# Kernel optimization log

Hardware: AMD Instinct MI355X
Metric: run time of the kernel (lower is better)

Reference implementation:

```python
import jax, jax.numpy as jnp
import numpy as np

B, N, FIN, D = 4, 16384, 128, 256
GX, GY = 32, 32
M = GX * GY
NBR = 1
K = (2 * NBR + 1) ** 2
IMG_W, IMG_H = 256.0, 256.0
CELL_W, CELL_H = IMG_W / GX, IMG_H / GY
EPS = 1e-5

# (K,2) offsets, row-major (-n,-n)..(n,n), [dx,dy] like torch _build_offsets_2d
_ys, _xs = np.meshgrid(np.arange(-NBR, NBR + 1), np.arange(-NBR, NBR + 1), indexing='ij')
OFFSETS = jnp.asarray(np.stack([_xs.ravel(), _ys.ravel()], axis=-1), dtype=jnp.int32)  # (K,2)


def setup_inputs() -> dict:
    key = jax.random.key(0)
    ks = jax.random.split(key, 16)
    s = 0.02
    return {
        'features': jax.random.normal(ks[0], (B, N, FIN), dtype=jnp.float32),
        'coords': jax.random.uniform(ks[1], (B, N, 2), dtype=jnp.float32) * IMG_W,
        'valid_mask': jnp.ones((B, N), dtype=bool),
        'Wf': jax.random.normal(ks[2], (FIN, D), dtype=jnp.float32) * s,
        'bf': jnp.zeros((D,), dtype=jnp.float32),
        'Wq': jax.random.normal(ks[3], (D, D), dtype=jnp.float32) * s,
        'bq': jnp.zeros((D,), dtype=jnp.float32),
        'Wk': jax.random.normal(ks[4], (D, D), dtype=jnp.float32) * s,
        'bk': jnp.zeros((D,), dtype=jnp.float32),
        'Wv': jax.random.normal(ks[5], (D, D), dtype=jnp.float32) * s,
        'bv': jnp.zeros((D,), dtype=jnp.float32),
        'Wo': jax.random.normal(ks[6], (D, D), dtype=jnp.float32) * s,
        'bo': jnp.zeros((D,), dtype=jnp.float32),
        'pos_emb': jax.random.normal(ks[7], (K, D), dtype=jnp.float32) * s,
        'gamma': jnp.ones((D,), dtype=jnp.float32),
        'beta': jnp.zeros((D,), dtype=jnp.float32),
    }


def _forward(features, coords, valid_mask, Wf, bf, Wq, bq, Wk, bk, Wv, bv, Wo, bo, pos_emb, gamma, beta):
    feat = features @ Wf + bf  # (B,N,D)

    # coords -> grid cell indices (truncation == torch .long() for nonneg coords)
    ix = jnp.clip((coords[..., 0] / CELL_W).astype(jnp.int32), 0, GX - 1)
    iy = jnp.clip((coords[..., 1] / CELL_H).astype(jnp.int32), 0, GY - 1)
    lin = ix * GY + iy  # (B,N)

    # scatter-mean pool into grid cells
    base = (jnp.arange(B, dtype=jnp.int32) * M)[:, None]
    gid = (lin + base).reshape(-1)  # (B*N,)
    pooled = jax.ops.segment_sum(feat.reshape(-1, D), gid, num_segments=B * M)
    cnt = jax.ops.segment_sum(jnp.ones((B * N,), feat.dtype), gid, num_segments=B * M)
    grid_flat = (pooled / jnp.maximum(cnt, 1.0)[:, None]).reshape(B, M, D)

    # neighbor gather with edge clamping + validity mask
    nbx = ix[:, :, None] + OFFSETS[None, None, :, 0]  # (B,N,K)
    nby = iy[:, :, None] + OFFSETS[None, None, :, 1]
    valid = (nbx >= 0) & (nbx < GX) & (nby >= 0) & (nby < GY)
    lin_n = jnp.clip(nbx, 0, GX - 1) * GY + jnp.clip(nby, 0, GY - 1)  # (B,N,K)
    nbr_feat = jnp.take_along_axis(grid_flat, lin_n.reshape(B, N * K, 1), axis=1).reshape(B, N, K, D)
    nbr_feat = nbr_feat + pos_emb[None, None, :, :]

    # tiny-window attention (1 query vs K neighbors); SDPA scale = 1/sqrt(D)
    Q = feat @ Wq + bq  # (B,N,D)
    Kt = nbr_feat @ Wk + bk  # (B,N,K,D)
    Vt = nbr_feat @ Wv + bv
    scores = jnp.einsum('bnd,bnkd->bnk', Q, Kt) / jnp.sqrt(jnp.float32(D))
    scores = jnp.where(valid, scores, -jnp.inf)
    attn = jax.nn.softmax(scores, axis=-1)
    out = jnp.einsum('bnk,bnkd->bnd', attn, Vt)
    out = out @ Wo + bo

    # residual + layernorm
    h = feat + out
    mu = jnp.mean(h, axis=-1, keepdims=True)
    var = jnp.var(h, axis=-1, keepdims=True)
    h = (h - mu) * jax.lax.rsqrt(var + EPS) * gamma + beta

    return jnp.where(valid_mask[..., None], h, feat)


def reference(features, coords, valid_mask, Wf, bf, Wq, bq, Wk, bk, Wv, bv, Wo, bo, pos_emb, gamma, beta):
    return _forward(features, coords, valid_mask, Wf, bf, Wq, bq, Wk, bk, Wv, bv, Wo, bo, pos_emb, gamma, beta)
```

## Files before the change

### kernel.cpp

```cpp
#include <hip/hip_runtime.h>
#include <math.h>

typedef _Float16 f16;
typedef _Float16 f16x8 __attribute__((ext_vector_type(8)));
typedef float f32x4 __attribute__((ext_vector_type(4)));

constexpr int cB   = 4;
constexpr int cN   = 16384;
constexpr int cFIN = 128;
constexpr int cD   = 256;
constexpr int cGX  = 32;
constexpr int cGY  = 32;
constexpr int cM   = cGX * cGY;
constexpr int cBM  = cB * cM;
constexpr int cBN  = cB * cN;
constexpr int cK   = 9;
constexpr float cEPS = 1e-5f;
constexpr int RPB  = 64;
constexpr int GSTR = 264;
constexpr int FSTR = 264;

struct f16pair { f16 h; f16 l; };
__device__ inline f16pair split2(float x) {
  f16pair p;
  p.h = (f16)x;
  p.l = (f16)(x - (float)p.h);
  return p;
}

__global__ __launch_bounds__(256)
void k_index(const float* __restrict__ coords, int* __restrict__ lin_arr,
             int* __restrict__ cntI) {
  int p = blockIdx.x * 256 + threadIdx.x;
  if (p >= cBN) return;
  float x = coords[2 * p], y = coords[2 * p + 1];
  int ix = (int)(x * 0.125f);
  int iy = (int)(y * 0.125f);
  ix = min(max(ix, 0), cGX - 1);
  iy = min(max(iy, 0), cGY - 1);
  int lin = ix * cGY + iy;
  lin_arr[p] = lin;
  int b = p / cN;
  atomicAdd(&cntI[b * cM + lin], 1);
}

__global__ __launch_bounds__(1024)
void k_scan(const int* __restrict__ cntI, int* __restrict__ bstart,
            int* __restrict__ bfill) {
  __shared__ int sums[1024];
  int t = threadIdx.x;
  int base = t * 4;
  int v0 = cntI[base], v1 = cntI[base + 1], v2 = cntI[base + 2], v3 = cntI[base + 3];
  sums[t] = v0 + v1 + v2 + v3;
  __syncthreads();
  for (int off = 1; off < 1024; off <<= 1) {
    int val = (t >= off) ? sums[t - off] : 0;
    __syncthreads();
    sums[t] += val;
    __syncthreads();
  }
  int run = (t == 0) ? 0 : sums[t - 1];
  bstart[base] = run;     bfill[base] = run;     run += v0;
  bstart[base + 1] = run; bfill[base + 1] = run; run += v1;
  bstart[base + 2] = run; bfill[base + 2] = run; run += v2;
  bstart[base + 3] = run; bfill[base + 3] = run; run += v3;
  if (t == 1023) bstart[4096] = run;
}

__global__ __launch_bounds__(256)
void k_scatteridx(const int* __restrict__ lin_arr, int* __restrict__ bfill,
                  int* __restrict__ sorted) {
  int p = blockIdx.x * 256 + threadIdx.x;
  if (p >= cBN) return;
  int b = p / cN;
  int gid = b * cM + lin_arr[p];
  int pos = atomicAdd(&bfill[gid], 1);
  sorted[pos] = p;
}

__global__ __launch_bounds__(256)
void k_precompute(const float* __restrict__ Wf, const float* __restrict__ Wq,
                  const float* __restrict__ Wv, const float* __restrict__ Wo,
                  const float* __restrict__ Wk, const float* __restrict__ pe,
                  const float* __restrict__ bf, const float* __restrict__ bq,
                  const float* __restrict__ bv, const float* __restrict__ bo,
                  const float* __restrict__ bk,
                  f16* __restrict__ BTh, f16* __restrict__ BTl,
                  f16* __restrict__ WvoTh, f16* __restrict__ WvoTl,
                  f16* __restrict__ WkTh, f16* __restrict__ WkTl,
                  float* __restrict__ bias2, float* __restrict__ bvo,
                  float* __restrict__ PK, float* __restrict__ PVO) {
  __shared__ float sA[cD];
  __shared__ float sB[cD];
  int bid = blockIdx.x, n = threadIdx.x;
  if (bid < cFIN) {
    int k = bid;
    f16pair pw = split2(Wf[k * cD + n]);
    BTh[n * cFIN + k] = pw.h; BTl[n * cFIN + k] = pw.l;
    float acc = 0.f;
    for (int c = 0; c < cD; c++) acc += Wf[k * cD + c] * Wq[c * cD + n];
    f16pair p = split2(acc);
    BTh[(256 + n) * cFIN + k] = p.h;
    BTl[(256 + n) * cFIN + k] = p.l;
  } else if (bid < cFIN + cD) {
    int k = bid - cFIN;
    float acc = 0.f;
    for (int c = 0; c < cD; c++) acc += Wv[k * cD + c] * Wo[c * cD + n];
    f16pair p = split2(acc);
    WvoTh[n * cD + k] = p.h;
    WvoTl[n * cD + k] = p.l;
  } else if (bid == cFIN + cD) {
    float aq = 0.f, ao = 0.f;
    for (int c = 0; c < cD; c++) {
      aq += bf[c] * Wq[c * cD + n];
      ao += bv[c] * Wo[c * cD + n];
    }
    bias2[n] = bf[n];
    bias2[256 + n] = aq + bq[n];
    bvo[n] = ao + bo[n];
  } else if (bid < cFIN + cD + 1 + cD) {
    int n2 = bid - (cFIN + cD + 1);
    f16pair p = split2(Wk[n * cD + n2]);
    WkTh[n2 * cD + n] = p.h;
    WkTl[n2 * cD + n] = p.l;
  } else {
    int k = bid - (cFIN + cD + 1 + cD);
    sA[n] = pe[k * cD + n];
    __syncthreads();
    float av = 0.f, ak = 0.f;
    for (int c = 0; c < cD; c++) {
      float pv = sA[c];
      av += pv * Wv[c * cD + n];
      ak += pv * Wk[c * cD + n];
    }
    sB[n] = av;
    PK[k * cD + n] = ak + bk[n];
    __syncthreads();
    float ao = 0.f;
    for (int c = 0; c < cD; c++) ao += sB[c] * Wo[c * cD + n];
    PVO[k * cD + n] = ao;
  }
}

__global__ __launch_bounds__(256)
void k_poolsum(const float* __restrict__ features, const int* __restrict__ sorted,
               const int* __restrict__ bstart, f16* __restrict__ Sh,
               f16* __restrict__ Sl, f16* __restrict__ Fh, f16* __restrict__ Fl) {
  __shared__ float Stmp[2][cFIN];
  int gid = blockIdx.x;
  int t = threadIdx.x;
  int half = t >> 7, ch = t & 127;
  int s0 = bstart[gid], s1 = bstart[gid + 1];
  float acc = 0.f;
  for (int i = s0 + half; i < s1; i += 2) {
    int srow = sorted[i];
    float v = features[(size_t)srow * cFIN + ch];
    acc += v;
    f16pair pp = split2(v);
    Fh[(size_t)srow * cFIN + ch] = pp.h;
    Fl[(size_t)srow * cFIN + ch] = pp.l;
  }
  Stmp[half][ch] = acc;
  __syncthreads();
  if (half == 0) {
    f16pair p = split2(Stmp[0][ch] + Stmp[1][ch]);
    Sh[(size_t)gid * cFIN + ch] = p.h;
    Sl[(size_t)gid * cFIN + ch] = p.l;
  }
}

__global__ __launch_bounds__(256)
void k_gemm_gkv(const f16* __restrict__ Sh, const f16* __restrict__ Sl,
                const f16* __restrict__ WfTh, const f16* __restrict__ WfTl,
                const float* __restrict__ bfp, const int* __restrict__ bstart,
                const f16* __restrict__ WkTh, const f16* __restrict__ WkTl,
                const f16* __restrict__ WvoTh, const f16* __restrict__ WvoTl,
                float* __restrict__ GK, float* __restrict__ GVO) {
  __shared__ f16 gshH[RPB * GSTR];
  __shared__ f16 gshL[RPB * GSTR];
  int t = threadIdx.x;
  int w = t >> 6, lane = t & 63;
  int q = lane >> 4, l = lane & 15;
  size_t row0 = (size_t)blockIdx.x * RPB;

  f32x4 acc[4][4];
#pragma unroll
  for (int rs = 0; rs < 4; rs++)
#pragma unroll
    for (int tc = 0; tc < 4; tc++) acc[rs][tc] = (f32x4){0.f, 0.f, 0.f, 0.f};

  for (int kk = 0; kk < cFIN; kk += 32) {
    f16x8 a_h[4], a_l[4];
#pragma unroll
    for (int rs = 0; rs < 4; rs++) {
      size_t aoff = (row0 + rs * 16 + l) * cFIN + q * 8 + kk;
      a_h[rs] = *(const f16x8*)(Sh + aoff);
      a_l[rs] = *(const f16x8*)(Sl + aoff);
    }
#pragma unroll
    for (int tc = 0; tc < 4; tc++) {
      size_t boff = (size_t)((w * 4 + tc) * 16 + l) * cFIN + q * 8 + kk;
      f16x8 bh = *(const f16x8*)(WfTh + boff);
      f16x8 bl = *(const f16x8*)(WfTl + boff);
#pragma unroll
      for (int rs = 0; rs < 4; rs++) {
        acc[rs][tc] = __builtin_amdgcn_mfma_f32_16x16x32_f16(a_h[rs], bh, acc[rs][tc], 0, 0, 0);
        acc[rs][tc] = __builtin_amdgcn_mfma_f32_16x16x32_f16(a_h[rs], bl, acc[rs][tc], 0, 0, 0);
        acc[rs][tc] = __builtin_amdgcn_mfma_f32_16x16x32_f16(a_l[rs], bh, acc[rs][tc], 0, 0, 0);
      }
    }
  }
#pragma unroll
  for (int tc = 0; tc < 4; tc++) {
    int col = (w * 4 + tc) * 16 + l;
    float bias = bfp[col];
#pragma unroll
    for (int rs = 0; rs < 4; rs++)
#pragma unroll
      for (int r = 0; r < 4; r++) {
        size_t row = row0 + rs * 16 + q * 4 + r;
        int lr = rs * 16 + q * 4 + r;
        int cnt = bstart[row + 1] - bstart[row];
        float g = (cnt > 0) ? (acc[rs][tc][r] / (float)cnt + bias) : 0.f;
        f16pair p = split2(g);
        gshH[lr * GSTR + col] = p.h;
        gshL[lr * GSTR + col] = p.l;
      }
  }
  __syncthreads();

  for (int sel = 0; sel < 2; sel++) {
    const f16* BTh = sel ? WvoTh : WkTh;
    const f16* BTl = sel ? WvoTl : WkTl;
    float* outp = sel ? GVO : GK;
#pragma unroll
    for (int rs = 0; rs < 4; rs++)
#pragma unroll
      for (int tc = 0; tc < 4; tc++) acc[rs][tc] = (f32x4){0.f, 0.f, 0.f, 0.f};
    for (int kk = 0; kk < cD; kk += 32) {
      f16x8 a_h[4], a_l[4];
#pragma unroll
      for (int rs = 0; rs < 4; rs++) {
        int aoff = (rs * 16 + l) * GSTR + q * 8 + kk;
        a_h[rs] = *(const f16x8*)(gshH + aoff);
        a_l[rs] = *(const f16x8*)(gshL + aoff);
      }
#pragma unroll
      for (int tc = 0; tc < 4; tc++) {
        size_t boff = (size_t)((w * 4 + tc) * 16 + l) * cD + q * 8 + kk;
        f16x8 bh = *(const f16x8*)(BTh + boff);
        f16x8 bl = *(const f16x8*)(BTl + boff);
#pragma unroll
        for (int rs = 0; rs < 4; rs++) {
          acc[rs][tc] = __builtin_amdgcn_mfma_f32_16x16x32_f16(a_h[rs], bh, acc[rs][tc], 0, 0, 0);
          acc[rs][tc] = __builtin_amdgcn_mfma_f32_16x16x32_f16(a_h[rs], bl, acc[rs][tc], 0, 0, 0);
          acc[rs][tc] = __builtin_amdgcn_mfma_f32_16x16x32_f16(a_l[rs], bh, acc[rs][tc], 0, 0, 0);
        }
      }
    }
#pragma unroll
    for (int tc = 0; tc < 4; tc++) {
      int col = (w * 4 + tc) * 16 + l;
#pragma unroll
      for (int rs = 0; rs < 4; rs++)
#pragma unroll
        for (int r = 0; r < 4; r++) {
          size_t row = row0 + rs * 16 + q * 4 + r;
          outp[row * cD + col] = acc[rs][tc][r];
        }
    }
  }
}

__global__ __launch_bounds__(256)
void k_gemmFQ(const f16* __restrict__ Fh, const f16* __restrict__ Fl,
              const f16* __restrict__ BTh, const f16* __restrict__ BTl,
              const float* __restrict__ bias2,
              float* __restrict__ feat_out, float* __restrict__ Qout) {
  __shared__ float sC[16 * FSTR];
  int y = blockIdx.y;
  int t = threadIdx.x;
  int w = t >> 6, lane = t & 63;
  int q = lane >> 4, l = lane & 15;
  size_t row0 = (size_t)blockIdx.x * RPB;
  float* outp = y ? Qout : feat_out;

  f32x4 acc[4][4];
#pragma unroll
  for (int rs = 0; rs < 4; rs++)
#pragma unroll
    for (int tc = 0; tc < 4; tc++) acc[rs][tc] = (f32x4){0.f, 0.f, 0.f, 0.f};

  for (int kk = 0; kk < cFIN; kk += 32) {
    f16x8 a_h[4], a_l[4];
#pragma unroll
    for (int rs = 0; rs < 4; rs++) {
      size_t aoff = (row0 + rs * 16 + l) * cFIN + q * 8 + kk;
      a_h[rs] = *(const f16x8*)(Fh + aoff);
      a_l[rs] = *(const f16x8*)(Fl + aoff);
    }
#pragma unroll
    for (int tc = 0; tc < 4; tc++) {
      int ct = y * 16 + w * 4 + tc;
      size_t boff = (size_t)(ct * 16 + l) * cFIN + q * 8 + kk;
      f16x8 bh = *(const f16x8*)(BTh + boff);
      f16x8 bl = *(const f16x8*)(BTl + boff);
#pragma unroll
      for (int rs = 0; rs < 4; rs++) {
        acc[rs][tc] = __builtin_amdgcn_mfma_f32_16x16x32_f16(a_h[rs], bh, acc[rs][tc], 0, 0, 0);
        acc[rs][tc] = __builtin_amdgcn_mfma_f32_16x16x32_f16(a_h[rs], bl, acc[rs][tc], 0, 0, 0);
        acc[rs][tc] = __builtin_amdgcn_mfma_f32_16x16x32_f16(a_l[rs], bh, acc[rs][tc], 0, 0, 0);
      }
    }
  }

#pragma unroll
  for (int rs = 0; rs < 4; rs++) {
    if (rs > 0) __syncthreads();
#pragma unroll
    for (int tc = 0; tc < 4; tc++) {
      int col = (w * 4 + tc) * 16 + l;
      float b = bias2[y * 256 + col];
#pragma unroll
      for (int r = 0; r < 4; r++)
        sC[(q * 4 + r) * FSTR + col] = acc[rs][tc][r] + b;
    }
    __syncthreads();
#pragma unroll
    for (int j = 0; j < 4; j++) {
      int idx = j * 256 + t;
      int lr = idx >> 6;
      int c4 = (idx & 63) * 4;
      *(float4*)&outp[(row0 + rs * 16 + lr) * cD + c4] =
          *(const float4*)&sC[lr * FSTR + c4];
    }
  }
}

__global__ __launch_bounds__(256)
void k_attn(const float* __restrict__ Qbuf, const float* __restrict__ GK,
            const float* __restrict__ GVO, const float* __restrict__ PK,
            const float* __restrict__ PVO, const int* __restrict__ sorted,
            const int* __restrict__ bstart, const float* __restrict__ bvop,
            const float* __restrict__ gammap, const float* __restrict__ betap,
            float* __restrict__ out) {
  __shared__ float KK[cK][cD];
  __shared__ float VV[cK][cD];
  int gid = blockIdx.x;
  int b = gid / cM;
  int lin = gid % cM;
  int ix = lin / cGY, iy = lin % cGY;
  int t = threadIdx.x;

  int vm = 0;
  for (int k = 0; k < cK; k++) {
    int dx = k % 3 - 1, dy = k / 3 - 1;
    int nx = ix + dx, ny = iy + dy;
    bool v = (nx >= 0 && nx < cGX && ny >= 0 && ny < cGY);
    if (v) vm |= (1 << k);
    int cx = min(max(nx, 0), cGX - 1);
    int cy = min(max(ny, 0), cGY - 1);
    size_t nlin = (size_t)(b * cM + cx * cGY + cy);
    KK[k][t] = GK[nlin * cD + t] + PK[k * cD + t];
    VV[k][t] = GVO[nlin * cD + t] + PVO[k * cD + t];
  }
  __syncthreads();

  int s0 = bstart[gid], s1 = bstart[gid + 1];
  int wv = t >> 6, lane = t & 63;
  float4 c4 = *(const float4*)&bvop[lane * 4];
  float4 g4 = *(const float4*)&gammap[lane * 4];
  float4 be4 = *(const float4*)&betap[lane * 4];

  int ip = s0 + wv;
  if (ip >= s1) return;
  int p = sorted[ip];
  size_t off0 = (size_t)p * cD + lane * 4;
  float4 q4 = *(const float4*)&Qbuf[off0];
  float4 f = *(const float4*)&out[off0];
  while (true) {
    int ipn = ip + 4;
    bool more = ipn < s1;
    int pn = 0; size_t offn = 0;
    float4 q4n = {0.f, 0.f, 0.f, 0.f}, fn = {0.f, 0.f, 0.f, 0.f};
    if (more) {
      pn = sorted[ipn];
      offn = (size_t)pn * cD + lane * 4;
      q4n = *(const float4*)&Qbuf[offn];
      fn = *(const float4*)&out[offn];
    }

    float sc[cK];
#pragma unroll
    for (int k = 0; k < cK; k++) {
      float4 kk = *(const float4*)&KK[k][lane * 4];
      sc[k] = q4.x * kk.x + q4.y * kk.y + q4.z * kk.z + q4.w * kk.w;
    }
#pragma unroll
    for (int off = 32; off > 0; off >>= 1)
#pragma unroll
      for (int k = 0; k < cK; k++) sc[k] += __shfl_xor(sc[k], off, 64);

    float mx = -1e30f;
#pragma unroll
    for (int k = 0; k < cK; k++)
      if ((vm >> k) & 1) mx = fmaxf(mx, sc[k] * 0.0625f);
    float e[cK], ssum = 0.f;
#pragma unroll
    for (int k = 0; k < cK; k++) {
      float v = ((vm >> k) & 1) ? __expf(sc[k] * 0.0625f - mx) : 0.f;
      e[k] = v; ssum += v;
    }
    float inv = 1.f / ssum;
    float4 o = {0.f, 0.f, 0.f, 0.f};
#pragma unroll
    for (int k = 0; k < cK; k++) {
      float a = e[k] * inv;
      float4 vv = *(const float4*)&VV[k][lane * 4];
      o.x += a * vv.x; o.y += a * vv.y; o.z += a * vv.z; o.w += a * vv.w;
    }
    float4 h;
    h.x = f.x + o.x + c4.x; h.y = f.y + o.y + c4.y;
    h.z = f.z + o.z + c4.z; h.w = f.w + o.w + c4.w;
    float s = h.x + h.y + h.z + h.w;
    float ss = h.x * h.x + h.y * h.y + h.z * h.z + h.w * h.w;
#pragma unroll
    for (int o2 = 32; o2 > 0; o2 >>= 1) {
      s += __shfl_xor(s, o2, 64);
      ss += __shfl_xor(ss, o2, 64);
    }
    float mu = s * (1.f / cD);
    float var = ss * (1.f / cD) - mu * mu;
    float rs = rsqrtf(var + cEPS);
    float4 r;
    r.x = (h.x - mu) * rs * g4.x + be4.x;
    r.y = (h.y - mu) * rs * g4.y + be4.y;
    r.z = (h.z - mu) * rs * g4.z + be4.z;
    r.w = (h.w - mu) * rs * g4.w + be4.w;
    *(float4*)&out[off0] = r;

    if (!more) break;
    ip = ipn; p = pn; off0 = offn; q4 = q4n; f = fn;
  }
}

extern "C" void kernel_launch(void* const* d_in, const int* in_sizes, int n_in,
                              void* d_out, int out_size, void* d_ws, size_t ws_size,
                              hipStream_t stream) {
  (void)in_sizes; (void)n_in; (void)out_size; (void)ws_size;
  const float* features = (const float*)d_in[0];
  const float* coords   = (const float*)d_in[1];
  const float* Wf = (const float*)d_in[3];
  const float* bf = (const float*)d_in[4];
  const float* Wq = (const float*)d_in[5];
  const float* bq = (const float*)d_in[6];
  const float* Wk = (const float*)d_in[7];
  const float* bk = (const float*)d_in[8];
  const float* Wv = (const float*)d_in[9];
  const float* bv = (const float*)d_in[10];
  const float* Wo = (const float*)d_in[11];
  const float* bo = (const float*)d_in[12];
  const float* pe = (const float*)d_in[13];
  const float* gm = (const float*)d_in[14];
  const float* bt = (const float*)d_in[15];
  float* out = (float*)d_out;

  char* ws = (char*)d_ws;
  size_t o = 0;
  auto take = [&](size_t bytes) -> void* {
    void* p = ws + o;
    o = (o + bytes + 255) & ~(size_t)255;
    return p;
  };
  int* lin_arr = (int*)take((size_t)cBN * 4);
  int* sorted  = (int*)take((size_t)cBN * 4);
  int* bstart  = (int*)take((size_t)(cBM + 1) * 4);
  int* bfill   = (int*)take((size_t)cBM * 4);
  int* cntI    = (int*)take((size_t)cBM * 4);
  float* GK    = (float*)take((size_t)cBM * cD * 4);
  float* GVO   = (float*)take((size_t)cBM * cD * 4);
  float* PK    = (float*)take((size_t)cK * cD * 4);
  float* PVO   = (float*)take((size_t)cK * cD * 4);
  float* Qbuf  = (float*)take((size_t)cBN * cD * 4);
  f16* Fh      = (f16*)take((size_t)cBN * cFIN * 2);
  f16* Fl      = (f16*)take((size_t)cBN * cFIN * 2);
  f16* BTh     = (f16*)take((size_t)512 * cFIN * 2);
  f16* BTl     = (f16*)take((size_t)512 * cFIN * 2);
  f16* WvoTh   = (f16*)take((size_t)cD * cD * 2);
  f16* WvoTl   = (f16*)take((size_t)cD * cD * 2);
  f16* WkTh    = (f16*)take((size_t)cD * cD * 2);
  f16* WkTl    = (f16*)take((size_t)cD * cD * 2);
  f16* Sh      = (f16*)take((size_t)cBM * cFIN * 2);
  f16* Sl      = (f16*)take((size_t)cBM * cFIN * 2);
  float* bias2 = (float*)take((size_t)512 * 4);
  float* bvo   = (float*)take((size_t)cD * 4);

  (void)hipMemsetAsync(cntI, 0, (size_t)cBM * 4, stream);

  k_index<<<cBN / 256, 256, 0, stream>>>(coords, lin_arr, cntI);
  k_scan<<<1, 1024, 0, stream>>>(cntI, bstart, bfill);
  k_scatteridx<<<cBN / 256, 256, 0, stream>>>(lin_arr, bfill, sorted);
  k_precompute<<<cFIN + cD + 1 + cD + cK, 256, 0, stream>>>(
      Wf, Wq, Wv, Wo, Wk, pe, bf, bq, bv, bo, bk,
      BTh, BTl, WvoTh, WvoTl, WkTh, WkTl, bias2, bvo, PK, PVO);
  k_poolsum<<<cBM, 256, 0, stream>>>(features, sorted, bstart, Sh, Sl, Fh, Fl);
  k_gemm_gkv<<<cBM / RPB, 256, 0, stream>>>(Sh, Sl, BTh, BTl, bf, bstart,
                                            WkTh, WkTl, WvoTh, WvoTl, GK, GVO);
  dim3 gFQ(cBN / RPB, 2);
  k_gemmFQ<<<gFQ, 256, 0, stream>>>(Fh, Fl, BTh, BTl, bias2, out, Qbuf);
  k_attn<<<cBM, 256, 0, stream>>>(Qbuf, GK, GVO, PK, PVO, sorted, bstart,
                                  bvo, gm, bt, out);
}
```

Before: 334.6 us.

## Shrink grid GEMM tiles, prefetch A in FQ GEMM, use half-wave rows in attention

The grid-cell GEMM now processes 16 rows per block instead of 64, giving 256 blocks instead of 64 so more CUs are busy on this small GEMM, at the cost of reloading weight tiles more often. The feature/Q GEMM double-buffers its A-operand loads across K steps to hide global latency. The attention kernel maps each point to a 32-lane half-wave handling 8 channels per lane, processing 8 points per block at a time with shorter shuffle reductions. The sC row stride padding also changes from 264 to 268.

```diff
diff --git a/kernel.cpp b/kernel.cpp
--- a/kernel.cpp
+++ b/kernel.cpp
@@ -17,8 +17,9 @@
 constexpr int cK   = 9;
 constexpr float cEPS = 1e-5f;
 constexpr int RPB  = 64;
+constexpr int RPG  = 16;
 constexpr int GSTR = 264;
-constexpr int FSTR = 264;
+constexpr int FSTR = 268;
 
 struct f16pair { f16 h; f16 l; };
 __device__ inline f16pair split2(float x) {
@@ -176,38 +177,29 @@
                 const f16* __restrict__ WkTh, const f16* __restrict__ WkTl,
                 const f16* __restrict__ WvoTh, const f16* __restrict__ WvoTl,
                 float* __restrict__ GK, float* __restrict__ GVO) {
-  __shared__ f16 gshH[RPB * GSTR];
-  __shared__ f16 gshL[RPB * GSTR];
+  __shared__ f16 gshH[RPG * GSTR];
+  __shared__ f16 gshL[RPG * GSTR];
   int t = threadIdx.x;
   int w = t >> 6, lane = t & 63;
   int q = lane >> 4, l = lane & 15;
-  size_t row0 = (size_t)blockIdx.x * RPB;
-
-  f32x4 acc[4][4];
-#pragma unroll
-  for (int rs = 0; rs < 4; rs++)
-#pragma unroll
-    for (int tc = 0; tc < 4; tc++) acc[rs][tc] = (f32x4){0.f, 0.f, 0.f, 0.f};
+  size_t row0 = (size_t)blockIdx.x * RPG;
+
+  f32x4 acc[4];
+#pragma unroll
+  for (int tc = 0; tc < 4; tc++) acc[tc] = (f32x4){0.f, 0.f, 0.f, 0.f};
 
   for (int kk = 0; kk < cFIN; kk += 32) {
-    f16x8 a_h[4], a_l[4];
-#pragma unroll
-    for (int rs = 0; rs < 4; rs++) {
-      size_t aoff = (row0 + rs * 16 + l) * cFIN + q * 8 + kk;
-      a_h[rs] = *(const f16x8*)(Sh + aoff);
-      a_l[rs] = *(const f16x8*)(Sl + aoff);
-    }
+    size_t aoff = (row0 + l) * cFIN + q * 8 + kk;
+    f16x8 a_h = *(const f16x8*)(Sh + aoff);
+    f16x8 a_l = *(const f16x8*)(Sl + aoff);
 #pragma unroll
     for (int tc = 0; tc < 4; tc++) {
       size_t boff = (size_t)((w * 4 + tc) * 16 + l) * cFIN + q * 8 + kk;
       f16x8 bh = *(const f16x8*)(WfTh + boff);
       f16x8 bl = *(const f16x8*)(WfTl + boff);
-#pragma unroll
-      for (int rs = 0; rs < 4; rs++) {
-        acc[rs][tc] = __builtin_amdgcn_mfma_f32_16x16x32_f16(a_h[rs], bh, acc[rs][tc], 0, 0, 0);
-        acc[rs][tc] = __builtin_amdgcn_mfma_f32_16x16x32_f16(a_h[rs], bl, acc[rs][tc], 0, 0, 0);
-        acc[rs][tc] = __builtin_amdgcn_mfma_f32_16x16x32_f16(a_l[rs], bh, acc[rs][tc], 0, 0, 0);
-      }
+      acc[tc] = __builtin_amdgcn_mfma_f32_16x16x32_f16(a_h, bh, acc[tc], 0, 0, 0);
+      acc[tc] = __builtin_amdgcn_mfma_f32_16x16x32_f16(a_h, bl, acc[tc], 0, 0, 0);
+      acc[tc] = __builtin_amdgcn_mfma_f32_16x16x32_f16(a_l, bh, acc[tc], 0, 0, 0);
     }
   }
 #pragma unroll
@@ -215,17 +207,15 @@
     int col = (w * 4 + tc) * 16 + l;
     float bias = bfp[col];
 #pragma unroll
-    for (int rs = 0; rs < 4; rs++)
-#pragma unroll
-      for (int r = 0; r < 4; r++) {
-        size_t row = row0 + rs * 16 + q * 4 + r;
-        int lr = rs * 16 + q * 4 + r;
-        int cnt = bstart[row + 1] - bstart[row];
-        float g = (cnt > 0) ? (acc[rs][tc][r] / (float)cnt + bias) : 0.f;
-        f16pair p = split2(g);
-        gshH[lr * GSTR + col] = p.h;
-        gshL[lr * GSTR + col] = p.l;
-      }
+    for (int r = 0; r < 4; r++) {
+      size_t row = row0 + q * 4 + r;
+      int lr = q * 4 + r;
+      int cnt = bstart[row + 1] - bstart[row];
+      float g = (cnt > 0) ? (acc[tc][r] / (float)cnt + bias) : 0.f;
+      f16pair p = split2(g);
+      gshH[lr * GSTR + col] = p.h;
+      gshL[lr * GSTR + col] = p.l;
+    }
   }
   __syncthreads();
 
@@ -234,40 +224,29 @@
     const f16* BTl = sel ? WvoTl : WkTl;
     float* outp = sel ? GVO : GK;
 #pragma unroll
-    for (int rs = 0; rs < 4; rs++)
-#pragma unroll
-      for (int tc = 0; tc < 4; tc++) acc[rs][tc] = (f32x4){0.f, 0.f, 0.f, 0.f};
+    for (int tc = 0; tc < 4; tc++) acc[tc] = (f32x4){0.f, 0.f, 0.f, 0.f};
     for (int kk = 0; kk < cD; kk += 32) {
-      f16x8 a_h[4], a_l[4];
-#pragma unroll
-      for (int rs = 0; rs < 4; rs++) {
-        int aoff = (rs * 16 + l) * GSTR + q * 8 + kk;
-        a_h[rs] = *(const f16x8*)(gshH + aoff);
-        a_l[rs] = *(const f16x8*)(gshL + aoff);
-      }
+      int aoff = l * GSTR + q * 8 + kk;
+      f16x8 a_h = *(const f16x8*)(gshH + aoff);
+      f16x8 a_l = *(const f16x8*)(gshL + aoff);
 #pragma unroll
       for (int tc = 0; tc < 4; tc++) {
         size_t boff = (size_t)((w * 4 + tc) * 16 + l) * cD + q * 8 + kk;
         f16x8 bh = *(const f16x8*)(BTh + boff);
         f16x8 bl = *(const f16x8*)(BTl + boff);
-#pragma unroll
-        for (int rs = 0; rs < 4; rs++) {
-          acc[rs][tc] = __builtin_amdgcn_mfma_f32_16x16x32_f16(a_h[rs], bh, acc[rs][tc], 0, 0, 0);
-          acc[rs][tc] = __builtin_amdgcn_mfma_f32_16x16x32_f16(a_h[rs], bl, acc[rs][tc], 0, 0, 0);
-          acc[rs][tc] = __builtin_amdgcn_mfma_f32_16x16x32_f16(a_l[rs], bh, acc[rs][tc], 0, 0, 0);
-        }
+        acc[tc] = __builtin_amdgcn_mfma_f32_16x16x32_f16(a_h, bh, acc[tc], 0, 0, 0);
+        acc[tc] = __builtin_amdgcn_mfma_f32_16x16x32_f16(a_h, bl, acc[tc], 0, 0, 0);
+        acc[tc] = __builtin_amdgcn_mfma_f32_16x16x32_f16(a_l, bh, acc[tc], 0, 0, 0);
       }
     }
 #pragma unroll
     for (int tc = 0; tc < 4; tc++) {
       int col = (w * 4 + tc) * 16 + l;
 #pragma unroll
-      for (int rs = 0; rs < 4; rs++)
-#pragma unroll
-        for (int r = 0; r < 4; r++) {
-          size_t row = row0 + rs * 16 + q * 4 + r;
-          outp[row * cD + col] = acc[rs][tc][r];
-        }
+      for (int r = 0; r < 4; r++) {
+        size_t row = row0 + q * 4 + r;
+        outp[row * cD + col] = acc[tc][r];
+      }
     }
   }
 }
@@ -291,13 +270,25 @@
 #pragma unroll
     for (int tc = 0; tc < 4; tc++) acc[rs][tc] = (f32x4){0.f, 0.f, 0.f, 0.f};
 
-  for (int kk = 0; kk < cFIN; kk += 32) {
-    f16x8 a_h[4], a_l[4];
-#pragma unroll
-    for (int rs = 0; rs < 4; rs++) {
-      size_t aoff = (row0 + rs * 16 + l) * cFIN + q * 8 + kk;
-      a_h[rs] = *(const f16x8*)(Fh + aoff);
-      a_l[rs] = *(const f16x8*)(Fl + aoff);
+  f16x8 a_h[4], a_l[4];
+#pragma unroll
+  for (int rs = 0; rs < 4; rs++) {
+    size_t aoff = (row0 + rs * 16 + l) * cFIN + q * 8;
+    a_h[rs] = *(const f16x8*)(Fh + aoff);
+    a_l[rs] = *(const f16x8*)(Fl + aoff);
+  }
+
+#pragma unroll
+  for (int step = 0; step < 4; step++) {
+    const int kk = step * 32;
+    f16x8 na_h[4], na_l[4];
+    if (step < 3) {
+#pragma unroll
+      for (int rs = 0; rs < 4; rs++) {
+        size_t aoff = (row0 + rs * 16 + l) * cFIN + q * 8 + kk + 32;
+        na_h[rs] = *(const f16x8*)(Fh + aoff);
+        na_l[rs] = *(const f16x8*)(Fl + aoff);
+      }
     }
 #pragma unroll
     for (int tc = 0; tc < 4; tc++) {
@@ -311,6 +302,10 @@
         acc[rs][tc] = __builtin_amdgcn_mfma_f32_16x16x32_f16(a_h[rs], bl, acc[rs][tc], 0, 0, 0);
         acc[rs][tc] = __builtin_amdgcn_mfma_f32_16x16x32_f16(a_l[rs], bh, acc[rs][tc], 0, 0, 0);
       }
+    }
+    if (step < 3) {
+#pragma unroll
+      for (int rs = 0; rs < 4; rs++) { a_h[rs] = na_h[rs]; a_l[rs] = na_l[rs]; }
     }
   }
 
@@ -367,39 +362,51 @@
   __syncthreads();
 
   int s0 = bstart[gid], s1 = bstart[gid + 1];
-  int wv = t >> 6, lane = t & 63;
-  float4 c4 = *(const float4*)&bvop[lane * 4];
-  float4 g4 = *(const float4*)&gammap[lane * 4];
-  float4 be4 = *(const float4*)&betap[lane * 4];
-
-  int ip = s0 + wv;
+  int hw = t >> 5;
+  int l32 = t & 31;
+  int ch8 = l32 * 8;
+  float4 c4a = *(const float4*)&bvop[ch8];
+  float4 c4b = *(const float4*)&bvop[ch8 + 4];
+  float4 g4a = *(const float4*)&gammap[ch8];
+  float4 g4b = *(const float4*)&gammap[ch8 + 4];
+  float4 be4a = *(const float4*)&betap[ch8];
+  float4 be4b = *(const float4*)&betap[ch8 + 4];
+
+  int ip = s0 + hw;
   if (ip >= s1) return;
   int p = sorted[ip];
-  size_t off0 = (size_t)p * cD + lane * 4;
-  float4 q4 = *(const float4*)&Qbuf[off0];
-  float4 f = *(const float4*)&out[off0];
+  size_t off0 = (size_t)p * cD + ch8;
+  float4 qa = *(const float4*)&Qbuf[off0];
+  float4 qb = *(const float4*)&Qbuf[off0 + 4];
+  float4 fa = *(const float4*)&out[off0];
+  float4 fb = *(const float4*)&out[off0 + 4];
   while (true) {
-    int ipn = ip + 4;
+    int ipn = ip + 8;
     bool more = ipn < s1;
     int pn = 0; size_t offn = 0;
-    float4 q4n = {0.f, 0.f, 0.f, 0.f}, fn = {0.f, 0.f, 0.f, 0.f};
+    float4 qan = {0.f, 0.f, 0.f, 0.f}, qbn = {0.f, 0.f, 0.f, 0.f};
+    float4 fan = {0.f, 0.f, 0.f, 0.f}, fbn = {0.f, 0.f, 0.f, 0.f};
     if (more) {
       pn = sorted[ipn];
-      offn = (size_t)pn * cD + lane * 4;
-      q4n = *(const float4*)&Qbuf[offn];
-      fn = *(const float4*)&out[offn];
+      offn = (size_t)pn * cD + ch8;
+      qan = *(const float4*)&Qbuf[offn];
+      qbn = *(const float4*)&Qbuf[offn + 4];
+      fan = *(const float4*)&out[offn];
+      fbn = *(const float4*)&out[offn + 4];
     }
 
     float sc[cK];
 #pragma unroll
     for (int k = 0; k < cK; k++) {
-      float4 kk = *(const float4*)&KK[k][lane * 4];
-      sc[k] = q4.x * kk.x + q4.y * kk.y + q4.z * kk.z + q4.w * kk.w;
-    }
-#pragma unroll
-    for (int off = 32; off > 0; off >>= 1)
-#pragma unroll
-      for (int k = 0; k < cK; k++) sc[k] += __shfl_xor(sc[k], off, 64);
+      float4 k0 = *(const float4*)&KK[k][ch8];
+      float4 k1 = *(const float4*)&KK[k][ch8 + 4];
+      sc[k] = qa.x * k0.x + qa.y * k0.y + qa.z * k0.z + qa.w * k0.w +
+              qb.x * k1.x + qb.y * k1.y + qb.z * k1.z + qb.w * k1.w;
+    }
+#pragma unroll
+    for (int off = 16; off > 0; off >>= 1)
+#pragma unroll
+      for (int k = 0; k < cK; k++) sc[k] += __shfl_xor(sc[k], off, 32);
 
     float mx = -1e30f;
 #pragma unroll
@@ -412,35 +419,46 @@
       e[k] = v; ssum += v;
     }
     float inv = 1.f / ssum;
-    float4 o = {0.f, 0.f, 0.f, 0.f};
+    float4 oa = {0.f, 0.f, 0.f, 0.f}, ob = {0.f, 0.f, 0.f, 0.f};
 #pragma unroll
     for (int k = 0; k < cK; k++) {
       float a = e[k] * inv;
-      float4 vv = *(const float4*)&VV[k][lane * 4];
-      o.x += a * vv.x; o.y += a * vv.y; o.z += a * vv.z; o.w += a * vv.w;
-    }
-    float4 h;
-    h.x = f.x + o.x + c4.x; h.y = f.y + o.y + c4.y;
-    h.z = f.z + o.z + c4.z; h.w = f.w + o.w + c4.w;
-    float s = h.x + h.y + h.z + h.w;
-    float ss = h.x * h.x + h.y * h.y + h.z * h.z + h.w * h.w;
-#pragma unroll
-    for (int o2 = 32; o2 > 0; o2 >>= 1) {
-      s += __shfl_xor(s, o2, 64);
-      ss += __shfl_xor(ss, o2, 64);
+      float4 v0 = *(const float4*)&VV[k][ch8];
+      float4 v1 = *(const float4*)&VV[k][ch8 + 4];
+      oa.x += a * v0.x; oa.y += a * v0.y; oa.z += a * v0.z; oa.w += a * v0.w;
+      ob.x += a * v1.x; ob.y += a * v1.y; ob.z += a * v1.z; ob.w += a * v1.w;
+    }
+    float4 ha, hb;
+    ha.x = fa.x + oa.x + c4a.x; ha.y = fa.y + oa.y + c4a.y;
+    ha.z = fa.z + oa.z + c4a.z; ha.w = fa.w + oa.w + c4a.w;
+    hb.x = fb.x + ob.x + c4b.x; hb.y = fb.y + ob.y + c4b.y;
+    hb.z = fb.z + ob.z + c4b.z; hb.w = fb.w + ob.w + c4b.w;
+    float s = ha.x + ha.y + ha.z + ha.w + hb.x + hb.y + hb.z + hb.w;
+    float ss = ha.x * ha.x + ha.y * ha.y + ha.z * ha.z + ha.w * ha.w +
+               hb.x * hb.x + hb.y * hb.y + hb.z * hb.z + hb.w * hb.w;
+#pragma unroll
+    for (int o2 = 16; o2 > 0; o2 >>= 1) {
+      s += __shfl_xor(s, o2, 32);
+      ss += __shfl_xor(ss, o2, 32);
     }
     float mu = s * (1.f / cD);
     float var = ss * (1.f / cD) - mu * mu;
-    float rs = rsqrtf(var + cEPS);
-    float4 r;
-    r.x = (h.x - mu) * rs * g4.x + be4.x;
-    r.y = (h.y - mu) * rs * g4.y + be4.y;
-    r.z = (h.z - mu) * rs * g4.z + be4.z;
-    r.w = (h.w - mu) * rs * g4.w + be4.w;
-    *(float4*)&out[off0] = r;
+    float rsr = rsqrtf(var + cEPS);
+    float4 ra, rb;
+    ra.x = (ha.x - mu) * rsr * g4a.x + be4a.x;
+    ra.y = (ha.y - mu) * rsr * g4a.y + be4a.y;
+    ra.z = (ha.z - mu) * rsr * g4a.z + be4a.z;
+    ra.w = (ha.w - mu) * rsr * g4a.w + be4a.w;
+    rb.x = (hb.x - mu) * rsr * g4b.x + be4b.x;
+    rb.y = (hb.y - mu) * rsr * g4b.y + be4b.y;
+    rb.z = (hb.z - mu) * rsr * g4b.z + be4b.z;
+    rb.w = (hb.w - mu) * rsr * g4b.w + be4b.w;
+    *(float4*)&out[off0] = ra;
+    *(float4*)&out[off0 + 4] = rb;
 
     if (!more) break;
-    ip = ipn; p = pn; off0 = offn; q4 = q4n; f = fn;
+    ip = ipn; p = pn; off0 = offn;
+    qa = qan; qb = qbn; fa = fan; fb = fbn;
   }
 }
 
@@ -504,7 +522,7 @@
       Wf, Wq, Wv, Wo, Wk, pe, bf, bq, bv, bo, bk,
       BTh, BTl, WvoTh, WvoTl, WkTh, WkTl, bias2, bvo, PK, PVO);
   k_poolsum<<<cBM, 256, 0, stream>>>(features, sorted, bstart, Sh, Sl, Fh, Fl);
-  k_gemm_gkv<<<cBM / RPB, 256, 0, stream>>>(Sh, Sl, BTh, BTl, bf, bstart,
+  k_gemm_gkv<<<cBM / RPG, 256, 0, stream>>>(Sh, Sl, BTh, BTl, bf, bstart,
                                             WkTh, WkTl, WvoTh, WvoTl, GK, GVO);
   dim3 gFQ(cBN / RPB, 2);
   k_gemmFQ<<<gFQ, 256, 0, stream>>>(Fh, Fl, BTh, BTl, bias2, out, Qbuf);
```

Result: faster. 321.7 us (-3.9%).
